# Performance work log

Measured on AMD Instinct MI355X. Metric: run time of the kernel, lower is better.

Reference implementation:

```python
import jax, jax.numpy as jnp
import numpy as np

INPLANES = 256
PLANES = 256
GROUPS = 4
B, N = 4, 2048
EPS = 1e-5


def setup_inputs() -> dict:
    key = jax.random.key(0)
    ks = jax.random.split(key, 8)
    s = 0.02
    return {
        "x": jax.random.normal(ks[0], (B, INPLANES, N), dtype=jnp.float32),
        "y": jax.random.normal(ks[1], (B, INPLANES, N), dtype=jnp.float32),
        # 1x1 Conv1d weights (out_ch, in_ch)
        "Wt": jax.random.normal(ks[2], (PLANES, INPLANES), dtype=jnp.float32) * s,
        "Wp": jax.random.normal(ks[3], (PLANES, INPLANES), dtype=jnp.float32) * s,
        "Wg": jax.random.normal(ks[4], (PLANES, INPLANES), dtype=jnp.float32) * s,
        # grouped 1x1 conv: (out_ch, in_ch/groups)
        "Wz": jax.random.normal(ks[5], (INPLANES, PLANES // GROUPS), dtype=jnp.float32) * s,
        # GroupNorm affine params
        "gamma": jnp.ones((INPLANES,), dtype=jnp.float32),
        "beta": jnp.zeros((INPLANES,), dtype=jnp.float32),
    }


def reference(x, y, Wt, Wp, Wg, Wz, gamma, beta):
    b, C, h = x.shape
    G = GROUPS
    P = Wt.shape[0]
    cg = P // G  # per-group channel dim

    # 1x1 convs == channel-mixing matmuls
    t = jnp.einsum('pc,bch->bph', Wt, y)  # values  [b,P,h]
    p = jnp.einsum('pc,bch->bph', Wp, x)  # queries [b,P,h]
    g = jnp.einsum('pc,bch->bph', Wg, y)  # keys    [b,P,h]

    # split channels into groups (vectorizes the per-group Python loop)
    tg = t.reshape(b, G, cg, h)
    pg = p.reshape(b, G, cg, h)
    gg = g.reshape(b, G, cg, h)

    # energy[b,g,i,j] = sum_c q[b,g,c,i] * k[b,g,c,j]   (no scaling in original)
    energy = jnp.einsum('bgci,bgcj->bgij', pg, gg)
    attn = jax.nn.softmax(energy, axis=-1)
    # out[b,g,c,i] = sum_j v[b,g,c,j] * attn[b,g,i,j]
    out = jnp.einsum('bgcj,bgij->bgci', tg, attn).reshape(b, P, h)

    # grouped 1x1 conv z: each group maps cg -> C/G channels
    Wzr = Wz.reshape(G, C // G, cg)
    z = jnp.einsum('god,bgdh->bgoh', Wzr, out.reshape(b, G, cg, h)).reshape(b, C, h)

    # GroupNorm over (channels-in-group, spatial)
    zg = z.reshape(b, G, -1)
    mean = jnp.mean(zg, axis=-1, keepdims=True)
    var = jnp.var(zg, axis=-1, keepdims=True)
    norm = ((zg - mean) * jax.lax.rsqrt(var + EPS)).reshape(b, C, h)
    return norm * gamma[None, :, None] + beta[None, :, None] + x
```

## Files before the change

### kernel.cpp

```cpp
#include <hip/hip_runtime.h>

typedef __attribute__((ext_vector_type(8))) short short8;
typedef __bf16 bf16x8 __attribute__((ext_vector_type(8)));
typedef __attribute__((ext_vector_type(4))) float f32x4;

static constexpr int Cn = 256, Nn = 2048;
static constexpr float EPSf = 1e-5f;
static constexpr float LOG2E = 1.44269504088896f;

#define DEV __device__ __forceinline__

DEV unsigned short f2bf(float f) { return __builtin_bit_cast(unsigned short, (__bf16)f); }
DEV float bf2f(unsigned u16) { return __builtin_bit_cast(float, u16 << 16); }
DEV unsigned pk2bf(float a, float b) {
  return (unsigned)f2bf(a) | ((unsigned)f2bf(b) << 16);
}
DEV f32x4 mfma16(short8 a, short8 b, f32x4 c) {
  return __builtin_amdgcn_mfma_f32_16x16x32_bf16(
      __builtin_bit_cast(bf16x8, a), __builtin_bit_cast(bf16x8, b), c, 0, 0, 0);
}
DEV short8 ld8(const unsigned short* p) { return *(const short8*)p; }

__global__ __launch_bounds__(256) void k_mix(
    const float* __restrict__ x, const float* __restrict__ y,
    const float* __restrict__ Wp, const float* __restrict__ Wt,
    const float* __restrict__ Wg, unsigned short* __restrict__ P,
    unsigned short* __restrict__ T, unsigned short* __restrict__ Gt,
    float* __restrict__ SUMS) {
  __shared__ __align__(16) unsigned short lds[12800];

  int t = threadIdx.x, lane = t & 63, w = t >> 6;
  int q = lane >> 4, li = lane & 15;
  int zb = blockIdx.y, b = zb & 3, op = zb >> 2;
  const float* in = (op == 0 ? x : y) + (size_t)b * Cn * Nn;
  const float* W = (op == 0 ? Wp : (op == 1 ? Wt : Wg));
  int h0 = blockIdx.x * 64;
  if (blockIdx.x == 0 && zb == 0) {
    SUMS[t] = 0.f;
    SUMS[256 + t] = 0.f;
  }

  int arow = t >> 3, ac4 = t & 7;
  int bcp = t >> 4, bh4 = t & 15;
  float4 wv[8], bv0, bv1;
#pragma unroll
  for (int i2 = 0; i2 < 8; ++i2)
    wv[i2] = *(const float4*)&W[(size_t)(i2 * 32 + arow) * 256 + ac4 * 4];
  bv0 = *(const float4*)&in[(size_t)(2 * bcp) * Nn + h0 + bh4 * 4];
  bv1 = *(const float4*)&in[(size_t)(2 * bcp + 1) * Nn + h0 + bh4 * 4];

  unsigned* bdst = (unsigned*)&lds[10240];
  f32x4 acc[4][4] = {};
  for (int kk = 0; kk < 8; ++kk) {
    __syncthreads();
#pragma unroll
    for (int i2 = 0; i2 < 8; ++i2)
      *(uint2*)&lds[(i2 * 32 + arow) * 40 + ac4 * 4] =
          make_uint2(pk2bf(wv[i2].x, wv[i2].y), pk2bf(wv[i2].z, wv[i2].w));
    {
      int hL = bh4 * 4;
      bdst[(hL + 0) * 20 + bcp] = pk2bf(bv0.x, bv1.x);
      bdst[(hL + 1) * 20 + bcp] = pk2bf(bv0.y, bv1.y);
      bdst[(hL + 2) * 20 + bcp] = pk2bf(bv0.z, bv1.z);
      bdst[(hL + 3) * 20 + bcp] = pk2bf(bv0.w, bv1.w);
    }
    if (kk < 7) {
      int k1 = (kk + 1) * 32;
#pragma unroll
      for (int i2 = 0; i2 < 8; ++i2)
        wv[i2] = *(const float4*)&W[(size_t)(i2 * 32 + arow) * 256 + k1 + ac4 * 4];
      bv0 = *(const float4*)&in[(size_t)(k1 + 2 * bcp) * Nn + h0 + bh4 * 4];
      bv1 = *(const float4*)&in[(size_t)(k1 + 2 * bcp + 1) * Nn + h0 + bh4 * 4];
    }
    __syncthreads();
    int pw = w * 64;
    short8 af[4];
#pragma unroll
    for (int mt = 0; mt < 4; ++mt)
      af[mt] = *(const short8*)&lds[(pw + mt * 16 + li) * 40 + q * 8];
#pragma unroll
    for (int nt = 0; nt < 4; ++nt) {
      short8 bfr = *(const short8*)&lds[10240 + (nt * 16 + li) * 40 + q * 8];
#pragma unroll
      for (int mt = 0; mt < 4; ++mt) acc[mt][nt] = mfma16(af[mt], bfr, acc[mt][nt]);
    }
  }
  int pw = w * 64;
  if (op < 2) {
    unsigned short* dst = (op == 0 ? P : T) + (size_t)b * Cn * Nn;
#pragma unroll
    for (int mt = 0; mt < 4; ++mt)
#pragma unroll
      for (int nt = 0; nt < 4; ++nt)
#pragma unroll
        for (int r = 0; r < 4; ++r)
          dst[(size_t)(pw + mt * 16 + q * 4 + r) * Nn + h0 + nt * 16 + li] =
              f2bf(acc[mt][nt][r]);
  } else {
#pragma unroll
    for (int mt = 0; mt < 4; ++mt)
#pragma unroll
      for (int nt = 0; nt < 4; ++nt)
#pragma unroll
        for (int r = 0; r < 4; ++r) {
          int c = pw + mt * 16 + q * 4 + r;
          int h = h0 + nt * 16 + li;
          Gt[(((size_t)(b * 4 + (c >> 6)) * Nn + h) << 6) + (c & 63)] =
              f2bf(acc[mt][nt][r] * LOG2E);
        }
  }
}

__global__ __launch_bounds__(256) void k_attn(
    const unsigned short* __restrict__ Pq, const unsigned short* __restrict__ Tv,
    const unsigned short* __restrict__ Gt, unsigned short* __restrict__ OT) {
  __shared__ __align__(16) unsigned short lds[16384];

  int t = threadIdx.x, lane = t & 63, w = t >> 6;
  int q = lane >> 4, li = lane & 15;
  int bid = blockIdx.x;
  int xcd = bid & 7, slot = bid >> 3;
  int bg = xcd * 2 + (slot >> 5);
  int i0 = (slot & 31) * 64;
  int b = bg >> 2, g = bg & 3;
  const unsigned short* Q = Pq + (size_t)(b * Cn + g * 64) * Nn;
  const unsigned short* V = Tv + (size_t)(b * Cn + g * 64) * Nn;
  const unsigned short* Kk = Gt + (size_t)bg * Nn * 64;

  int iw = i0 + w * 16;
  short8 qf[2];
#pragma unroll
  for (int cs = 0; cs < 2; ++cs) {
    short8 v;
#pragma unroll
    for (int e = 0; e < 8; ++e)
      v[e] = (short)Q[(size_t)(cs * 32 + q * 8 + e) * Nn + iw + li];
    qf[cs] = v;
  }
  f32x4 O[4] = {};
  float rs = 0.f;

  int swz = li & 7;
  int rb0 = li * 64 + ((q ^ swz) << 3);
  int rb1 = li * 64 + (((4 + q) ^ swz) << 3);
  int srow = t >> 2, sq = t & 3;
  int wk0 = srow * 64 + ((sq ^ (srow & 7)) << 3);
  int wk1 = srow * 64 + (((sq + 4) ^ (srow & 7)) << 3);

  const unsigned short* kp0 = Kk + srow * 64 + sq * 8;
  const unsigned short* kp1 = kp0 + 32;
  const unsigned short* vp0 = V + (size_t)srow * Nn + sq * 8;
  const unsigned short* vp1 = vp0 + 32;

  short8 kst[2], vst[2];
  kst[0] = ld8(kp0); kst[1] = ld8(kp1);
  vst[0] = ld8(vp0); vst[1] = ld8(vp1);
  kp0 += 4096; kp1 += 4096; vp0 += 64; vp1 += 64;

  auto load_next = [&]() {
    kst[0] = ld8(kp0); kst[1] = ld8(kp1);
    vst[0] = ld8(vp0); vst[1] = ld8(vp1);
    kp0 += 4096; kp1 += 4096; vp0 += 64; vp1 += 64;
  };

  auto stage = [&](int KB) {
    *(short8*)&lds[KB + wk0] = kst[0];
    *(short8*)&lds[KB + wk1] = kst[1];
    *(short8*)&lds[KB + 8192 + wk0] = vst[0];
    *(short8*)&lds[KB + 8192 + wk1] = vst[1];
  };

  auto compute = [&](int KB) {
    f32x4 F[4] = {};
#pragma unroll
    for (int jt = 0; jt < 4; ++jt) {
      short8 k0 = *(const short8*)&lds[KB + jt * 1024 + rb0];
      short8 k1 = *(const short8*)&lds[KB + jt * 1024 + rb1];
      F[jt] = mfma16(k0, qf[0], F[jt]);
      F[jt] = mfma16(k1, qf[1], F[jt]);
    }
    unsigned pa[4], pb[4];
#pragma unroll
    for (int jt = 0; jt < 4; ++jt) {
      float e0 = __builtin_amdgcn_exp2f(F[jt][0]);
      float e1 = __builtin_amdgcn_exp2f(F[jt][1]);
      float e2 = __builtin_amdgcn_exp2f(F[jt][2]);
      float e3 = __builtin_amdgcn_exp2f(F[jt][3]);
      rs += (e0 + e1) + (e2 + e3);
      pa[jt] = pk2bf(e0, e1);
      pb[jt] = pk2bf(e2, e3);
    }
#pragma unroll
    for (int cs = 0; cs < 2; ++cs) {
      unsigned a0 = pa[2 * cs], a1 = pa[2 * cs + 1];
      unsigned b0 = pb[2 * cs], b1 = pb[2 * cs + 1];
      asm("v_permlane32_swap_b32 %0, %1" : "+v"(a0), "+v"(a1));
      asm("v_permlane16_swap_b32 %0, %1" : "+v"(a0), "+v"(a1));
      asm("v_permlane32_swap_b32 %0, %1" : "+v"(b0), "+v"(b1));
      asm("v_permlane16_swap_b32 %0, %1" : "+v"(b0), "+v"(b1));
      int4 fi = make_int4((int)a0, (int)b0, (int)a1, (int)b1);
      short8 pf = __builtin_bit_cast(short8, fi);
      int rbv = cs ? rb1 : rb0;
#pragma unroll
      for (int ct = 0; ct < 4; ++ct) {
        short8 vf = *(const short8*)&lds[KB + 8192 + ct * 1024 + rbv];
        O[ct] = mfma16(pf, vf, O[ct]);
      }
    }
  };

  for (int tp = 0; tp < 16; ++tp) {
    __syncthreads();
    stage(0);
    load_next();
    if (tp > 0) compute(4096);
    __syncthreads();
    stage(4096);
    if (tp < 15) load_next();
    compute(0);
  }
  __syncthreads();
  compute(4096);

  rs += __shfl_xor(rs, 16);
  rs += __shfl_xor(rs, 32);
  float r0 = 1.f / __shfl(rs, q * 4 + 0);
  float r1 = 1.f / __shfl(rs, q * 4 + 1);
  float r2 = 1.f / __shfl(rs, q * 4 + 2);
  float r3 = 1.f / __shfl(rs, q * 4 + 3);
  unsigned short* op = OT + (size_t)bg * Nn * 64;
#pragma unroll
  for (int ct = 0; ct < 4; ++ct) {
    op[(size_t)(iw + q * 4 + 0) * 64 + ct * 16 + li] = f2bf(O[ct][0] * r0);
    op[(size_t)(iw + q * 4 + 1) * 64 + ct * 16 + li] = f2bf(O[ct][1] * r1);
    op[(size_t)(iw + q * 4 + 2) * 64 + ct * 16 + li] = f2bf(O[ct][2] * r2);
    op[(size_t)(iw + q * 4 + 3) * 64 + ct * 16 + li] = f2bf(O[ct][3] * r3);
  }
}

__global__ __launch_bounds__(256) void k_zconv(
    const float* __restrict__ Wz, const unsigned short* __restrict__ OT,
    unsigned short* __restrict__ Zb, float* __restrict__ SUMS) {
  __shared__ __align__(16) unsigned short lds[8192];
  __shared__ float red[8];
  int t = threadIdx.x, lane = t & 63, w = t >> 6;
  int q = lane >> 4, li = lane & 15;
  int bg = blockIdx.y, b = bg >> 2, g = bg & 3;
  int i0 = blockIdx.x * 64;
  const unsigned short* region = OT + ((size_t)bg * Nn + i0) * 64;
#pragma unroll
  for (int p = 0; p < 2; ++p) {
    int chunk = p * 256 + t;
    int row = chunk >> 3, sl = chunk & 7;
    short8 v = ld8(region + row * 64 + sl * 8);
    *(short8*)&lds[row * 64 + (sl ^ (row & 7)) * 8] = v;
  }
  const float* Wg2 = Wz + g * 64 * 64;
#pragma unroll
  for (int p = 0; p < 4; ++p) {
    int o = p * 16 + (t >> 4), f4c = t & 15;
    float4 v = *(const float4*)&Wg2[o * 64 + f4c * 4];
    *(uint2*)&lds[4096 + o * 64 + ((f4c >> 1) ^ (o & 7)) * 8 + (f4c & 1) * 4] =
        make_uint2(pk2bf(v.x, v.y), pk2bf(v.z, v.w));
  }
  __syncthreads();
  f32x4 acc[4] = {};
#pragma unroll
  for (int cs = 0; cs < 2; ++cs) {
    int hrow = w * 16 + li;
    short8 bfr = *(const short8*)&lds[hrow * 64 + ((cs * 4 + q) ^ (hrow & 7)) * 8];
#pragma unroll
    for (int mt = 0; mt < 4; ++mt) {
      int orow = mt * 16 + li;
      short8 af =
          *(const short8*)&lds[4096 + orow * 64 + ((cs * 4 + q) ^ (orow & 7)) * 8];
      acc[mt] = mfma16(af, bfr, acc[mt]);
    }
  }
  float s1 = 0.f, s2 = 0.f;
  unsigned short* zb = Zb + (size_t)(b * Cn + g * 64) * Nn;
#pragma unroll
  for (int mt = 0; mt < 4; ++mt)
#pragma unroll
    for (int r = 0; r < 4; ++r) {
      float v = acc[mt][r];
      s1 += v; s2 += v * v;
      zb[(size_t)(mt * 16 + q * 4 + r) * Nn + i0 + w * 16 + li] = f2bf(v);
    }
#pragma unroll
  for (int off = 32; off; off >>= 1) {
    s1 += __shfl_xor(s1, off);
    s2 += __shfl_xor(s2, off);
  }
  if (lane == 0) { red[w * 2] = s1; red[w * 2 + 1] = s2; }
  __syncthreads();
  if (t == 0) {
    float a1 = red[0] + red[2] + red[4] + red[6];
    float a2 = red[1] + red[3] + red[5] + red[7];
    atomicAdd(&SUMS[bg * 32], a1);
    atomicAdd(&SUMS[bg * 32 + 1], a2);
  }
}

__global__ __launch_bounds__(256) void k_norm(
    const unsigned short* __restrict__ Zb, const float* __restrict__ x,
    const float* __restrict__ gamma, const float* __restrict__ beta,
    const float* __restrict__ SUMS, float* __restrict__ out) {
  int idx = blockIdx.x * 256 + threadIdx.x;
  size_t f = (size_t)idx * 4;
  int c = (int)((f >> 11) & (Cn - 1));
  int b = (int)(f >> 19);
  int bg = b * 4 + (c >> 6);
  const float inv = 1.f / 131072.f;
  float mean = SUMS[bg * 32] * inv;
  float var = SUMS[bg * 32 + 1] * inv - mean * mean;
  float rstd = rsqrtf(var + EPSf);
  float ga = gamma[c] * rstd;
  float be = beta[c] - mean * ga;
  uint2 u = *(const uint2*)&Zb[f];
  float4 xv = *(const float4*)(x + f);
  float4 o;
  o.x = bf2f(u.x & 0xffffu) * ga + be + xv.x;
  o.y = bf2f(u.x >> 16) * ga + be + xv.y;
  o.z = bf2f(u.y & 0xffffu) * ga + be + xv.z;
  o.w = bf2f(u.y >> 16) * ga + be + xv.w;
  *(float4*)(out + f) = o;
}

extern "C" void kernel_launch(void* const* d_in, const int* in_sizes, int n_in,
                              void* d_out, int out_size, void* d_ws, size_t ws_size,
                              hipStream_t stream) {
  (void)in_sizes; (void)n_in; (void)out_size; (void)ws_size;
  const float* x = (const float*)d_in[0];
  const float* y = (const float*)d_in[1];
  const float* Wt = (const float*)d_in[2];
  const float* Wp = (const float*)d_in[3];
  const float* Wg = (const float*)d_in[4];
  const float* Wz = (const float*)d_in[5];
  const float* gamma = (const float*)d_in[6];
  const float* beta = (const float*)d_in[7];
  float* out = (float*)d_out;
  char* ws = (char*)d_ws;
  unsigned short* Pq = (unsigned short*)(ws + 0);
  unsigned short* Tv = (unsigned short*)(ws + 4194304);
  unsigned short* Gt = (unsigned short*)(ws + 8388608);
  unsigned short* OT = (unsigned short*)(ws + 12582912);
  unsigned short* Zb = (unsigned short*)(ws + 16777216);
  float* SUMS = (float*)(ws + 20971520);

  k_mix<<<dim3(32, 12), 256, 0, stream>>>(x, y, Wp, Wt, Wg, Pq, Tv, Gt, SUMS);
  k_attn<<<512, 256, 0, stream>>>(Pq, Tv, Gt, OT);
  k_zconv<<<dim3(32, 16), 256, 0, stream>>>(Wz, OT, Zb, SUMS);
  k_norm<<<2048, 256, 0, stream>>>(Zb, x, gamma, beta, SUMS, out);
}
```

Before: 59.48 us.

## Split attention key range across two blocks and merge partials in zconv

Each attention block now processes half of the key positions, doubling the grid to improve CU occupancy and latency hiding. Each half writes its normalized partial output in bf16 plus its row sums. The z-conv kernel reweights and merges the two partials by their row sums before the matmul. This costs extra global traffic for the second partial buffer and an added bf16 rounding step. The Zb workspace now aliases the Pq buffer.

```diff
diff --git a/kernel.cpp b/kernel.cpp
--- a/kernel.cpp
+++ b/kernel.cpp
@@ -113,15 +113,19 @@
 
 __global__ __launch_bounds__(256) void k_attn(
     const unsigned short* __restrict__ Pq, const unsigned short* __restrict__ Tv,
-    const unsigned short* __restrict__ Gt, unsigned short* __restrict__ OT) {
+    const unsigned short* __restrict__ Gt, unsigned short* __restrict__ PO0,
+    unsigned short* __restrict__ PO1, float* __restrict__ RS) {
   __shared__ __align__(16) unsigned short lds[16384];
 
   int t = threadIdx.x, lane = t & 63, w = t >> 6;
   int q = lane >> 4, li = lane & 15;
   int bid = blockIdx.x;
   int xcd = bid & 7, slot = bid >> 3;
-  int bg = xcd * 2 + (slot >> 5);
-  int i0 = (slot & 31) * 64;
+  int bg = xcd * 2 + (slot >> 6);
+  int rem = slot & 63;
+  int half = rem >> 5;
+  int i0 = (rem & 31) * 64;
+  int jbase = half * 1024;
   int b = bg >> 2, g = bg & 3;
   const unsigned short* Q = Pq + (size_t)(b * Cn + g * 64) * Nn;
   const unsigned short* V = Tv + (size_t)(b * Cn + g * 64) * Nn;
@@ -147,9 +151,9 @@
   int wk0 = srow * 64 + ((sq ^ (srow & 7)) << 3);
   int wk1 = srow * 64 + (((sq + 4) ^ (srow & 7)) << 3);
 
-  const unsigned short* kp0 = Kk + srow * 64 + sq * 8;
+  const unsigned short* kp0 = Kk + (size_t)(jbase + srow) * 64 + sq * 8;
   const unsigned short* kp1 = kp0 + 32;
-  const unsigned short* vp0 = V + (size_t)srow * Nn + sq * 8;
+  const unsigned short* vp0 = V + (size_t)srow * Nn + jbase + sq * 8;
   const unsigned short* vp1 = vp0 + 32;
 
   short8 kst[2], vst[2];
@@ -209,14 +213,14 @@
     }
   };
 
-  for (int tp = 0; tp < 16; ++tp) {
+  for (int tp = 0; tp < 8; ++tp) {
     __syncthreads();
     stage(0);
     load_next();
     if (tp > 0) compute(4096);
     __syncthreads();
     stage(4096);
-    if (tp < 15) load_next();
+    if (tp < 7) load_next();
     compute(0);
   }
   __syncthreads();
@@ -224,22 +228,24 @@
 
   rs += __shfl_xor(rs, 16);
   rs += __shfl_xor(rs, 32);
+  if (q == 0) RS[(size_t)(half * 16 + bg) * Nn + iw + li] = rs;
   float r0 = 1.f / __shfl(rs, q * 4 + 0);
   float r1 = 1.f / __shfl(rs, q * 4 + 1);
   float r2 = 1.f / __shfl(rs, q * 4 + 2);
   float r3 = 1.f / __shfl(rs, q * 4 + 3);
-  unsigned short* op = OT + (size_t)bg * Nn * 64;
+  unsigned short* PO = (half ? PO1 : PO0) + (size_t)bg * Nn * 64;
 #pragma unroll
   for (int ct = 0; ct < 4; ++ct) {
-    op[(size_t)(iw + q * 4 + 0) * 64 + ct * 16 + li] = f2bf(O[ct][0] * r0);
-    op[(size_t)(iw + q * 4 + 1) * 64 + ct * 16 + li] = f2bf(O[ct][1] * r1);
-    op[(size_t)(iw + q * 4 + 2) * 64 + ct * 16 + li] = f2bf(O[ct][2] * r2);
-    op[(size_t)(iw + q * 4 + 3) * 64 + ct * 16 + li] = f2bf(O[ct][3] * r3);
+    PO[(size_t)(iw + q * 4 + 0) * 64 + ct * 16 + li] = f2bf(O[ct][0] * r0);
+    PO[(size_t)(iw + q * 4 + 1) * 64 + ct * 16 + li] = f2bf(O[ct][1] * r1);
+    PO[(size_t)(iw + q * 4 + 2) * 64 + ct * 16 + li] = f2bf(O[ct][2] * r2);
+    PO[(size_t)(iw + q * 4 + 3) * 64 + ct * 16 + li] = f2bf(O[ct][3] * r3);
   }
 }
 
 __global__ __launch_bounds__(256) void k_zconv(
-    const float* __restrict__ Wz, const unsigned short* __restrict__ OT,
+    const float* __restrict__ Wz, const unsigned short* __restrict__ PO0,
+    const unsigned short* __restrict__ PO1, const float* __restrict__ RS,
     unsigned short* __restrict__ Zb, float* __restrict__ SUMS) {
   __shared__ __align__(16) unsigned short lds[8192];
   __shared__ float red[8];
@@ -247,13 +253,25 @@
   int q = lane >> 4, li = lane & 15;
   int bg = blockIdx.y, b = bg >> 2, g = bg & 3;
   int i0 = blockIdx.x * 64;
-  const unsigned short* region = OT + ((size_t)bg * Nn + i0) * 64;
+  const unsigned short* po0 = PO0 + ((size_t)bg * Nn + i0) * 64;
+  const unsigned short* po1 = PO1 + ((size_t)bg * Nn + i0) * 64;
+  const float* rs0p = RS + (size_t)bg * Nn + i0;
+  const float* rs1p = RS + (size_t)(16 + bg) * Nn + i0;
 #pragma unroll
   for (int p = 0; p < 2; ++p) {
     int chunk = p * 256 + t;
     int row = chunk >> 3, sl = chunk & 7;
-    short8 v = ld8(region + row * 64 + sl * 8);
-    *(short8*)&lds[row * 64 + (sl ^ (row & 7)) * 8] = v;
+    short8 a = ld8(po0 + row * 64 + sl * 8);
+    short8 bb = ld8(po1 + row * 64 + sl * 8);
+    float ra = rs0p[row], rb = rs1p[row];
+    float inv = 1.f / (ra + rb);
+    float w0 = ra * inv, w1 = rb * inv;
+    short8 m;
+#pragma unroll
+    for (int e = 0; e < 8; ++e)
+      m[e] = (short)f2bf(bf2f((unsigned short)a[e]) * w0 +
+                         bf2f((unsigned short)bb[e]) * w1);
+    *(short8*)&lds[row * 64 + (sl ^ (row & 7)) * 8] = m;
   }
   const float* Wg2 = Wz + g * 64 * 64;
 #pragma unroll
@@ -341,15 +359,17 @@
   const float* beta = (const float*)d_in[7];
   float* out = (float*)d_out;
   char* ws = (char*)d_ws;
-  unsigned short* Pq = (unsigned short*)(ws + 0);
-  unsigned short* Tv = (unsigned short*)(ws + 4194304);
-  unsigned short* Gt = (unsigned short*)(ws + 8388608);
-  unsigned short* OT = (unsigned short*)(ws + 12582912);
-  unsigned short* Zb = (unsigned short*)(ws + 16777216);
-  float* SUMS = (float*)(ws + 20971520);
+  unsigned short* Pq  = (unsigned short*)(ws + 0);
+  unsigned short* Tv  = (unsigned short*)(ws + 4194304);
+  unsigned short* Gt  = (unsigned short*)(ws + 8388608);
+  unsigned short* PO0 = (unsigned short*)(ws + 12582912);
+  unsigned short* PO1 = (unsigned short*)(ws + 16777216);
+  float* RS   = (float*)(ws + 20971520);
+  float* SUMS = (float*)(ws + 21233664);
+  unsigned short* Zb = Pq;
 
   k_mix<<<dim3(32, 12), 256, 0, stream>>>(x, y, Wp, Wt, Wg, Pq, Tv, Gt, SUMS);
-  k_attn<<<512, 256, 0, stream>>>(Pq, Tv, Gt, OT);
-  k_zconv<<<dim3(32, 16), 256, 0, stream>>>(Wz, OT, Zb, SUMS);
+  k_attn<<<1024, 256, 0, stream>>>(Pq, Tv, Gt, PO0, PO1, RS);
+  k_zconv<<<dim3(32, 16), 256, 0, stream>>>(Wz, PO0, PO1, RS, Zb, SUMS);
   k_norm<<<2048, 256, 0, stream>>>(Zb, x, gamma, beta, SUMS, out);
 }
```

After: 58.38 us. Within noise of the previous version (-1.8%).
